# Optimization experiments

Measured on AMD Instinct MI355X. Metric: run time of the kernel, lower is better.

## Reference

```python
import jax, jax.numpy as jnp
import numpy as np

STATE_DIM, ACTION_DIM, HIDDEN_DIM = 512, 64, 2048
INPUT_DIM = STATE_DIM + ACTION_DIM + 1  # 577
BATCH = 4096


def setup_inputs() -> dict:
    key = jax.random.key(0)
    ks = jax.random.split(key, 12)
    sc_x = 1.0 / np.sqrt(INPUT_DIM)
    sc_h = 1.0 / np.sqrt(HIDDEN_DIM)
    return {
        "s": jax.random.normal(ks[0], (BATCH, STATE_DIM), jnp.float32),
        "a_prev": jax.random.normal(ks[1], (BATCH, ACTION_DIM), jnp.float32),
        "r_prev": jax.random.normal(ks[2], (BATCH, 1), jnp.float32),
        "h": jnp.zeros((HIDDEN_DIM,), jnp.float32),
        "c": jnp.zeros((HIDDEN_DIM,), jnp.float32),
        # Fused gate weights: columns ordered [i, f, g(c-tilde), o]
        "Wx": jax.random.uniform(ks[3], (INPUT_DIM, 4 * HIDDEN_DIM), jnp.float32, -sc_x, sc_x),
        "Wh": jax.random.uniform(ks[4], (HIDDEN_DIM, 4 * HIDDEN_DIM), jnp.float32, -sc_h, sc_h),
        "bh": jax.random.uniform(ks[5], (4 * HIDDEN_DIM,), jnp.float32, -sc_h, sc_h),
        "Wa": jax.random.uniform(ks[6], (HIDDEN_DIM, ACTION_DIM), jnp.float32, -sc_h, sc_h),
        "ba": jax.random.uniform(ks[7], (ACTION_DIM,), jnp.float32, -sc_h, sc_h),
        "Wv": jax.random.uniform(ks[8], (HIDDEN_DIM, 1), jnp.float32, -sc_h, sc_h),
        "bv": jax.random.uniform(ks[9], (1,), jnp.float32, -sc_h, sc_h),
    }


def reference(s, a_prev, r_prev, h, c, Wx, Wh, bh, Wa, ba, Wv, bv):
    # x: [B, input_dim]
    x = jnp.concatenate([s, a_prev, r_prev], axis=1)
    # Two fused GEMMs replace the 8 separate small linears (same math).
    z = x @ Wx + h @ Wh + bh          # [B, 4H]
    zi, zf, zg, zo = jnp.split(z, 4, axis=-1)
    i = jax.nn.sigmoid(zi)
    f = jax.nn.sigmoid(zf)
    c_new = f * c + i * jnp.tanh(zg)  # [B, H] (c broadcast over batch)
    o = jax.nn.sigmoid(zo)
    h_new = o * jnp.tanh(c_new)       # [B, H]
    probs = jax.nn.softmax(h_new @ Wa + ba, axis=1)  # [B, A]
    v = h_new @ Wv + bv               # [B, 1]
    return (probs, v)
```

## Files before the change

kernel.cpp:

```cpp
#include <hip/hip_runtime.h>
#include <hip/hip_bf16.h>

#define BATCH   4096
#define SDIM    512
#define ADIM    64
#define IDIM    577
#define KP2     576
#define NKT64   9
#define HDIM    2048
#define ZDIM    8192
#define BUFE    (128 * 64)

typedef __attribute__((ext_vector_type(8))) __bf16 bf16x8;
typedef __attribute__((ext_vector_type(4))) __bf16 bf16x4;
typedef __attribute__((ext_vector_type(4))) float  accx4;

__global__ __launch_bounds__(256) void setup_kernel(
    const float* __restrict__ s, const float* __restrict__ a_prev,
    const float* __restrict__ h,
    const float* __restrict__ wx, const float* __restrict__ wh,
    const float* __restrict__ wa,
    __hip_bfloat16* __restrict__ xb, __hip_bfloat16* __restrict__ wxt,
    __hip_bfloat16* __restrict__ waT, float* __restrict__ zh_w)
{
    __shared__ float stile[64 * 65];
    const int bid = blockIdx.x;
    const int t = threadIdx.x;

    if (bid < 1152) {
        const int kt2 = bid >> 7;
        const int nt  = bid & 127;
        const int c4  = t & 15;
        const int rr  = t >> 4;
#pragma unroll
        for (int i = 0; i < 4; ++i) {
            const int r = rr + i * 16;
            const int k = kt2 * 64 + r;
            float4 v =
                *(const float4*)(wx + (size_t)k * ZDIM + nt * 64 + c4 * 4);
            *(float4*)(stile + r * 65 + c4 * 4) = v;
        }
        __syncthreads();
        const int ch = t & 7;
#pragma unroll
        for (int i = 0; i < 2; ++i) {
            const int nr = (t >> 3) + i * 32;
            bf16x8 w8;
#pragma unroll
            for (int j = 0; j < 8; ++j)
                w8[j] = (__bf16)stile[(ch * 8 + j) * 65 + nr];
            *(bf16x8*)(wxt + (size_t)(nt * 64 + nr) * KP2 + kt2 * 64 + ch * 8)
                = w8;
        }
    } else if (bid < 2176) {
        const int zb = bid - 1152;
        const int nb = zb & 63, ky = zb >> 6;
        const int n  = nb * 128 + (t & 127);
        const int kh = t >> 7;
        const float* hp  = h + ky * 128 + kh * 64;
        const float* whp = wh + (size_t)(ky * 128 + kh * 64) * ZDIM + n;
        float p = 0.0f;
#pragma unroll 32
        for (int kk = 0; kk < 64; ++kk)
            p = fmaf(hp[kk], whp[(size_t)kk * ZDIM], p);
        stile[t] = p;
        __syncthreads();
        if (t < 128)
            zh_w[ky * ZDIM + n] = stile[t] + stile[t + 128];
    } else if (bid < 2432) {
        const int row0 = (bid - 2176) * 16;
        const int tr = t >> 4, tc = t & 15;
        const int row = row0 + tr;
        const float* srow = s + (size_t)row * SDIM;
        const float* arow = a_prev + (size_t)row * ADIM;
        __hip_bfloat16* xrow = xb + (size_t)row * KP2;
#pragma unroll
        for (int j = 0; j < 9; ++j) {
            const int c4  = j * 16 + tc;
            const int col = c4 * 4;
            float4 v = (col < SDIM)
                ? *(const float4*)(srow + col)
                : *(const float4*)(arow + (col - SDIM));
            bf16x4 w;
            w[0] = (__bf16)v.x; w[1] = (__bf16)v.y;
            w[2] = (__bf16)v.z; w[3] = (__bf16)v.w;
            *(bf16x4*)(xrow + col) = w;
        }
    } else {
        const int wb = bid - 2432;
        const int kt = wb >> 1, at = wb & 1;
        const int c  = t & 31, r0 = t >> 5;
#pragma unroll
        for (int i = 0; i < 4; ++i) {
            int r = r0 + i * 8;
            stile[r * 33 + c] = wa[(size_t)(kt * 32 + r) * ADIM + at * 32 + c];
        }
        __syncthreads();
#pragma unroll
        for (int i = 0; i < 4; ++i) {
            int r = r0 + i * 8;
            waT[(size_t)(at * 32 + r) * HDIM + kt * 32 + c] =
                __float2bfloat16(stile[c * 33 + r]);
        }
    }
}

__device__ __forceinline__ float rcp_f(float x) {
    return __builtin_amdgcn_rcpf(x);
}
__device__ __forceinline__ float sigmoid_f(float x) {
    return rcp_f(1.0f + __expf(-x));
}
__device__ __forceinline__ float tanh_f(float x) {
    return 1.0f - 2.0f * rcp_f(1.0f + __expf(2.0f * x));
}

__global__ __launch_bounds__(256, 2) void lstm_gemm(
    const __hip_bfloat16* __restrict__ xb,
    const __hip_bfloat16* __restrict__ wxt,
    const float* __restrict__ zh_w,
    const float* __restrict__ bh,
    const float* __restrict__ cvec,
    const float* __restrict__ wx,
    const float* __restrict__ r_prev,
    __hip_bfloat16* __restrict__ hout)
{
    __shared__ __bf16 smA[2 * BUFE];
    __shared__ __bf16 smB[2 * BUFE];
    const int t    = threadIdx.x;
    const int lane = t & 63;
    const int wid  = t >> 6;
    const int m0   = blockIdx.x * 128;
    const int n0   = blockIdx.y * 32;
    const int wm   = wid >> 1, wn = wid & 1;
    const int fl15 = lane & 15;
    const int fhi  = lane >> 4;

    accx4 acc[4][4] = {};

    const int srow = lane >> 3;
    const int slot = lane & 7;
    const int cch  = slot ^ srow;
    const __bf16* gA[4]; const __bf16* gB[4]; int lofs[4];
#pragma unroll
    for (int i = 0; i < 4; ++i) {
        const int r = wid * 32 + i * 8 + srow;
        gA[i] = (const __bf16*)xb + (size_t)(m0 + r) * KP2 + cch * 8;
        const int g = r >> 5, nn = r & 31;
        gB[i] = (const __bf16*)wxt +
                (size_t)(g * HDIM + n0 + nn) * KP2 + cch * 8;
        lofs[i] = (wid * 32 + i * 8) * 64;
    }

    auto stage = [&](int tile, int p) {
        const int ko = tile * 64;
        const int po = p * BUFE;
#pragma unroll
        for (int i = 0; i < 4; ++i) {
            __builtin_amdgcn_global_load_lds(
                (const __attribute__((address_space(1))) void*)(gA[i] + ko),
                (__attribute__((address_space(3))) void*)(smA + po + lofs[i]),
                16, 0, 0);
            __builtin_amdgcn_global_load_lds(
                (const __attribute__((address_space(1))) void*)(gB[i] + ko),
                (__attribute__((address_space(3))) void*)(smB + po + lofs[i]),
                16, 0, 0);
        }
    };

    auto compute = [&](int p) {
        const int po = p * BUFE;
#pragma unroll
        for (int hf = 0; hf < 2; ++hf) {
            const int ck = hf * 4 + fhi;
            const int sl = (ck ^ (fl15 & 7)) * 8;
            bf16x8 af[4], bfr[4];
#pragma unroll
            for (int rt = 0; rt < 4; ++rt)
                af[rt] = *(const bf16x8*)(smA + po +
                    (wm * 64 + rt * 16 + fl15) * 64 + sl);
#pragma unroll
            for (int g = 0; g < 4; ++g)
                bfr[g] = *(const bf16x8*)(smB + po +
                    (g * 32 + wn * 16 + fl15) * 64 + sl);
#pragma unroll
            for (int g = 0; g < 4; ++g)
#pragma unroll
                for (int rt = 0; rt < 4; ++rt)
                    acc[g][rt] = __builtin_amdgcn_mfma_f32_16x16x32_bf16(
                        af[rt], bfr[g], acc[g][rt], 0, 0, 0);
        }
    };

    stage(0, 0);
    asm volatile("s_waitcnt vmcnt(0)" ::: "memory");
    __builtin_amdgcn_s_barrier();
#pragma unroll
    for (int kt = 0; kt < NKT64 - 1; ++kt) {
        stage(kt + 1, (kt + 1) & 1);
        asm volatile("s_waitcnt vmcnt(8)" ::: "memory");
        __builtin_amdgcn_s_barrier();
        compute(kt & 1);
        __builtin_amdgcn_s_barrier();
    }
    asm volatile("s_waitcnt vmcnt(0)" ::: "memory");
    __builtin_amdgcn_s_barrier();
    compute((NKT64 - 1) & 1);

    const int colg = n0 + wn * 16 + fl15;
    float zsum[4], wxr[4];
#pragma unroll
    for (int g = 0; g < 4; ++g) {
        float z = bh[g * HDIM + colg];
#pragma unroll
        for (int j = 0; j < 16; ++j)
            z += zh_w[j * ZDIM + g * HDIM + colg];
        zsum[g] = z;
        wxr[g] = wx[(size_t)576 * ZDIM + g * HDIM + colg];
    }
    const float cv = cvec[colg];
#pragma unroll
    for (int rt = 0; rt < 4; ++rt) {
#pragma unroll
        for (int r = 0; r < 4; ++r) {
            const int row = m0 + wm * 64 + rt * 16 + (fhi << 2) + r;
            const float rv = r_prev[row];
            const float zi = acc[0][rt][r] + zsum[0] + rv * wxr[0];
            const float zf = acc[1][rt][r] + zsum[1] + rv * wxr[1];
            const float zg = acc[2][rt][r] + zsum[2] + rv * wxr[2];
            const float zo = acc[3][rt][r] + zsum[3] + rv * wxr[3];
            const float cn = sigmoid_f(zf) * cv + sigmoid_f(zi) * tanh_f(zg);
            const float hn = sigmoid_f(zo) * tanh_f(cn);
            hout[(size_t)row * HDIM + colg] = __float2bfloat16(hn);
        }
    }
}

__global__ __launch_bounds__(512) void head_kernel(
    const __hip_bfloat16* __restrict__ hnew,
    const __hip_bfloat16* __restrict__ waT,
    const float* __restrict__ wv,
    const float* __restrict__ ba, const float* __restrict__ bv,
    float* __restrict__ probs, float* __restrict__ vout)
{
    __shared__ float lg[8][16][68];
    __shared__ float vpart[8][16];
    const int t    = threadIdx.x;
    const int lane = t & 63;
    const int w    = t >> 6;
    const int r0   = blockIdx.x * 16;
    const int fl15 = lane & 15, fhi = lane >> 4;
    const int k0   = w * 256;

    const __bf16* arow = (const __bf16*)hnew +
        (size_t)(r0 + fl15) * HDIM + k0 + fhi * 8;
    const __bf16* brow = (const __bf16*)waT +
        (size_t)fl15 * HDIM + k0 + fhi * 8;
    const float* wvp = wv + k0 + fhi * 8;

    accx4 acc[4] = {};
    float va0 = 0.f, va1 = 0.f;
#pragma unroll
    for (int kk = 0; kk < 256; kk += 32) {
        bf16x8 af = *(const bf16x8*)(arow + kk);
#pragma unroll
        for (int a = 0; a < 4; ++a) {
            bf16x8 bf = *(const bf16x8*)(brow + (size_t)a * 16 * HDIM + kk);
            acc[a] = __builtin_amdgcn_mfma_f32_16x16x32_bf16(
                af, bf, acc[a], 0, 0, 0);
        }
#pragma unroll
        for (int j = 0; j < 4; ++j) {
            va0 = fmaf((float)af[j],     wvp[kk + j],     va0);
            va1 = fmaf((float)af[j + 4], wvp[kk + j + 4], va1);
        }
    }
#pragma unroll
    for (int a = 0; a < 4; ++a)
#pragma unroll
        for (int r = 0; r < 4; ++r)
            lg[w][fhi * 4 + r][a * 16 + fl15] = acc[a][r];
    float va = va0 + va1;
    va += __shfl_xor(va, 16);
    va += __shfl_xor(va, 32);
    if (lane < 16) vpart[w][lane] = va;
    __syncthreads();

    const float bav = ba[lane];
#pragma unroll
    for (int i = 0; i < 2; ++i) {
        const int row = w * 2 + i;
        float logit = bav;
#pragma unroll
        for (int p = 0; p < 8; ++p)
            logit += lg[p][row][lane];
        float m = logit;
#pragma unroll
        for (int mask = 32; mask >= 1; mask >>= 1)
            m = fmaxf(m, __shfl_xor(m, mask));
        const float e = __expf(logit - m);
        float ssum = e;
#pragma unroll
        for (int mask = 32; mask >= 1; mask >>= 1)
            ssum += __shfl_xor(ssum, mask);
        probs[(size_t)(r0 + row) * 64 + lane] = e / ssum;
    }
    if (t < 16) {
        float v = bv[0];
#pragma unroll
        for (int p = 0; p < 8; ++p)
            v += vpart[p][t];
        vout[r0 + t] = v;
    }
}

extern "C" void kernel_launch(void* const* d_in, const int* in_sizes, int n_in,
                              void* d_out, int out_size, void* d_ws,
                              size_t ws_size, hipStream_t stream)
{
    const float* s      = (const float*)d_in[0];
    const float* a_prev = (const float*)d_in[1];
    const float* r_prev = (const float*)d_in[2];
    const float* h      = (const float*)d_in[3];
    const float* c      = (const float*)d_in[4];
    const float* Wx     = (const float*)d_in[5];
    const float* Wh     = (const float*)d_in[6];
    const float* bh     = (const float*)d_in[7];
    const float* Wa     = (const float*)d_in[8];
    const float* ba     = (const float*)d_in[9];
    const float* Wv     = (const float*)d_in[10];
    const float* bv     = (const float*)d_in[11];

    float* out   = (float*)d_out;
    float* probs = out;
    float* vout  = out + (size_t)BATCH * ADIM;

    char* ws = (char*)d_ws;
    __hip_bfloat16* xb   = (__hip_bfloat16*)ws;
    __hip_bfloat16* wxt  = (__hip_bfloat16*)(ws + 4718592);
    __hip_bfloat16* waT  = (__hip_bfloat16*)(ws + 14155776);
    float* zh_w          = (float*)(ws + 14417920);
    __hip_bfloat16* hnew = (__hip_bfloat16*)(ws + 14942208);

    setup_kernel<<<2560, 256, 0, stream>>>(
        s, a_prev, h, Wx, Wh, Wa, xb, wxt, waT, zh_w);
    lstm_gemm<<<dim3(BATCH / 128, HDIM / 32), 256, 0, stream>>>(
        xb, wxt, zh_w, bh, c, Wx, r_prev, hnew);
    head_kernel<<<BATCH / 16, 512, 0, stream>>>(
        hnew, waT, Wv, ba, bv, probs, vout);
}
```

Before: 198.4 us.

## Enlarge LSTM GEMM M-tile to 256 rows with 32-wide K steps

The fused gate GEMM's block tile grows from 128 to 256 batch rows, with each wave now holding 8x4 accumulator fragments. The K step drops from 64 to 32, giving 18 pipeline iterations, and the LDS swizzle changes to fit the 32-wide rows. Each loaded weight tile is now reused across twice as many rows, which halves B-operand global traffic and the grid size. In exchange, register pressure rises (128 accumulator floats per lane), there are twice as many barriers per K pass, and fewer blocks are available to fill the GPU.

```diff
diff --git a/kernel.cpp b/kernel.cpp
--- a/kernel.cpp
+++ b/kernel.cpp
@@ -6,10 +6,11 @@
 #define ADIM    64
 #define IDIM    577
 #define KP2     576
-#define NKT64   9
+#define NKT32   18
 #define HDIM    2048
 #define ZDIM    8192
-#define BUFE    (128 * 64)
+#define AELEM   (256 * 32)
+#define BELEM   (128 * 32)
 
 typedef __attribute__((ext_vector_type(8))) __bf16 bf16x8;
 typedef __attribute__((ext_vector_type(4))) __bf16 bf16x4;
@@ -125,70 +126,74 @@
     const float* __restrict__ r_prev,
     __hip_bfloat16* __restrict__ hout)
 {
-    __shared__ __bf16 smA[2 * BUFE];
-    __shared__ __bf16 smB[2 * BUFE];
+    __shared__ __bf16 smA[2 * AELEM];
+    __shared__ __bf16 smB[2 * BELEM];
     const int t    = threadIdx.x;
     const int lane = t & 63;
     const int wid  = t >> 6;
-    const int m0   = blockIdx.x * 128;
+    const int m0   = blockIdx.x * 256;
     const int n0   = blockIdx.y * 32;
-    const int wm   = wid >> 1, wn = wid & 1;
+    const int wm   = wid >> 1;
+    const int wn   = wid & 1;
     const int fl15 = lane & 15;
     const int fhi  = lane >> 4;
 
-    accx4 acc[4][4] = {};
-
-    const int srow = lane >> 3;
-    const int slot = lane & 7;
-    const int cch  = slot ^ srow;
-    const __bf16* gA[4]; const __bf16* gB[4]; int lofs[4];
+    accx4 acc[4][8] = {};
+
+    const int lrow = lane >> 2;
+    const int cch  = (lane & 3) ^ ((lane >> 3) & 3);
+    const __bf16* gA[4]; int lofsA[4];
+    const __bf16* gB[2]; int lofsB[2];
 #pragma unroll
     for (int i = 0; i < 4; ++i) {
-        const int r = wid * 32 + i * 8 + srow;
-        gA[i] = (const __bf16*)xb + (size_t)(m0 + r) * KP2 + cch * 8;
-        const int g = r >> 5, nn = r & 31;
+        const int rA = wid * 64 + i * 16 + lrow;
+        gA[i] = (const __bf16*)xb + (size_t)(m0 + rA) * KP2 + cch * 8;
+        lofsA[i] = (wid * 64 + i * 16) * 32;
+    }
+#pragma unroll
+    for (int i = 0; i < 2; ++i) {
+        const int rB = wid * 32 + i * 16 + lrow;
+        const int g = rB >> 5, c = rB & 31;
         gB[i] = (const __bf16*)wxt +
-                (size_t)(g * HDIM + n0 + nn) * KP2 + cch * 8;
-        lofs[i] = (wid * 32 + i * 8) * 64;
+                (size_t)(g * HDIM + n0 + c) * KP2 + cch * 8;
+        lofsB[i] = (wid * 32 + i * 16) * 32;
     }
 
     auto stage = [&](int tile, int p) {
-        const int ko = tile * 64;
-        const int po = p * BUFE;
-#pragma unroll
-        for (int i = 0; i < 4; ++i) {
+        const int ko = tile * 32;
+#pragma unroll
+        for (int i = 0; i < 4; ++i)
             __builtin_amdgcn_global_load_lds(
                 (const __attribute__((address_space(1))) void*)(gA[i] + ko),
-                (__attribute__((address_space(3))) void*)(smA + po + lofs[i]),
+                (__attribute__((address_space(3))) void*)(smA + p * AELEM +
+                                                          lofsA[i]),
                 16, 0, 0);
+#pragma unroll
+        for (int i = 0; i < 2; ++i)
             __builtin_amdgcn_global_load_lds(
                 (const __attribute__((address_space(1))) void*)(gB[i] + ko),
-                (__attribute__((address_space(3))) void*)(smB + po + lofs[i]),
+                (__attribute__((address_space(3))) void*)(smB + p * BELEM +
+                                                          lofsB[i]),
                 16, 0, 0);
-        }
     };
 
+    const int sl = (fhi ^ ((fl15 >> 1) & 3)) * 8;
+
     auto compute = [&](int p) {
-        const int po = p * BUFE;
-#pragma unroll
-        for (int hf = 0; hf < 2; ++hf) {
-            const int ck = hf * 4 + fhi;
-            const int sl = (ck ^ (fl15 & 7)) * 8;
-            bf16x8 af[4], bfr[4];
-#pragma unroll
-            for (int rt = 0; rt < 4; ++rt)
-                af[rt] = *(const bf16x8*)(smA + po +
-                    (wm * 64 + rt * 16 + fl15) * 64 + sl);
+        const int poA = p * AELEM, poB = p * BELEM;
+        bf16x8 bfr[4];
+#pragma unroll
+        for (int g = 0; g < 4; ++g)
+            bfr[g] = *(const bf16x8*)(smB + poB +
+                (g * 32 + wn * 16 + fl15) * 32 + sl);
+#pragma unroll
+        for (int rt = 0; rt < 8; ++rt) {
+            bf16x8 af = *(const bf16x8*)(smA + poA +
+                (wm * 128 + rt * 16 + fl15) * 32 + sl);
 #pragma unroll
             for (int g = 0; g < 4; ++g)
-                bfr[g] = *(const bf16x8*)(smB + po +
-                    (g * 32 + wn * 16 + fl15) * 64 + sl);
-#pragma unroll
-            for (int g = 0; g < 4; ++g)
-#pragma unroll
-                for (int rt = 0; rt < 4; ++rt)
-                    acc[g][rt] = __builtin_amdgcn_mfma_f32_16x16x32_bf16(
-                        af[rt], bfr[g], acc[g][rt], 0, 0, 0);
+                acc[g][rt] = __builtin_amdgcn_mfma_f32_16x16x32_bf16(
+                    af, bfr[g], acc[g][rt], 0, 0, 0);
         }
     };
 
@@ -196,16 +201,16 @@
     asm volatile("s_waitcnt vmcnt(0)" ::: "memory");
     __builtin_amdgcn_s_barrier();
 #pragma unroll
-    for (int kt = 0; kt < NKT64 - 1; ++kt) {
+    for (int kt = 0; kt < NKT32 - 1; ++kt) {
         stage(kt + 1, (kt + 1) & 1);
-        asm volatile("s_waitcnt vmcnt(8)" ::: "memory");
+        asm volatile("s_waitcnt vmcnt(6)" ::: "memory");
         __builtin_amdgcn_s_barrier();
         compute(kt & 1);
         __builtin_amdgcn_s_barrier();
     }
     asm volatile("s_waitcnt vmcnt(0)" ::: "memory");
     __builtin_amdgcn_s_barrier();
-    compute((NKT64 - 1) & 1);
+    compute((NKT32 - 1) & 1);
 
     const int colg = n0 + wn * 16 + fl15;
     float zsum[4], wxr[4];
@@ -220,10 +225,10 @@
     }
     const float cv = cvec[colg];
 #pragma unroll
-    for (int rt = 0; rt < 4; ++rt) {
+    for (int rt = 0; rt < 8; ++rt) {
 #pragma unroll
         for (int r = 0; r < 4; ++r) {
-            const int row = m0 + wm * 64 + rt * 16 + (fhi << 2) + r;
+            const int row = m0 + wm * 128 + rt * 16 + (fhi << 2) + r;
             const float rv = r_prev[row];
             const float zi = acc[0][rt][r] + zsum[0] + rv * wxr[0];
             const float zf = acc[1][rt][r] + zsum[1] + rv * wxr[1];
@@ -344,7 +349,7 @@
 
     setup_kernel<<<2560, 256, 0, stream>>>(
         s, a_prev, h, Wx, Wh, Wa, xb, wxt, waT, zh_w);
-    lstm_gemm<<<dim3(BATCH / 128, HDIM / 32), 256, 0, stream>>>(
+    lstm_gemm<<<dim3(BATCH / 256, HDIM / 32), 256, 0, stream>>>(
         xb, wxt, zh_w, bh, c, Wx, r_prev, hnew);
     head_kernel<<<BATCH / 16, 512, 0, stream>>>(
         hnew, waT, Wv, ba, bv, probs, vout);
```

Result: no change. 202.0 us (+1.8%).
